# Optimization experiments

Hardware: AMD Instinct MI355X
Metric: run time of the kernel (lower is better)

## Reference

```python
import jax, jax.numpy as jnp
import numpy as np

FACTOR = 2
ALPHA = 0.1


def zero_upsample(x, f):
    # conv_transpose2d with one-hot (f,f) depthwise kernel == strided scatter
    N, C, H, W = x.shape
    out = jnp.zeros((N, C, H * f, W * f), dtype=x.dtype)
    return out.at[:, :, ::f, ::f].set(x)


def jitter_align(img, jitter, f):
    # pad by f on all sides (zeros), then per-batch crop shifted by floor(jitter*f)
    N, C, H, W = img.shape
    pad = jnp.pad(img, ((0, 0), (0, 0), (f, f), (f, f)))
    ji = jnp.floor(jitter * f).astype(jnp.int32)  # [N,2] = (x, y)
    def crop(im, jxy):
        i, j = jxy[1], jxy[0]
        return jax.lax.dynamic_slice(im, (0, f - i, f - j), (C, H, W))
    return jax.vmap(crop)(pad, ji)


def bilinear_upsample_jittered(img, jitter, f):
    # F.affine_grid(identity + translation) + grid_sample(bilinear,
    # align_corners=False, padding_mode='border')
    N, C, H, W = img.shape
    Ho, Wo = H * f, W * f
    xs = (2.0 * jnp.arange(Wo, dtype=img.dtype) + 1.0) / Wo - 1.0  # output pixel centers
    ys = (2.0 * jnp.arange(Ho, dtype=img.dtype) + 1.0) / Ho - 1.0
    def sample_one(im, jit):
        gx = xs + 2.0 * (0.5 - jit[0]) / W          # normalized grid x [Wo]
        gy = ys + 2.0 * (0.5 - jit[1]) / H          # normalized grid y [Ho]
        ix = ((gx + 1.0) * W - 1.0) / 2.0           # input pixel coords
        iy = ((gy + 1.0) * H - 1.0) / 2.0
        x0 = jnp.floor(ix)
        y0 = jnp.floor(iy)
        wx = (ix - x0)[None, None, :]               # [1,1,Wo]
        wy = (iy - y0)[None, :, None]               # [1,Ho,1]
        x0i = x0.astype(jnp.int32)
        y0i = y0.astype(jnp.int32)
        x0c = jnp.clip(x0i, 0, W - 1)
        x1c = jnp.clip(x0i + 1, 0, W - 1)
        y0c = jnp.clip(y0i, 0, H - 1)
        y1c = jnp.clip(y0i + 1, 0, H - 1)
        r0 = im[:, y0c, :]                          # [C,Ho,W]
        r1 = im[:, y1c, :]
        v00 = r0[:, :, x0c]; v01 = r0[:, :, x1c]    # [C,Ho,Wo]
        v10 = r1[:, :, x0c]; v11 = r1[:, :, x1c]
        top = v00 * (1 - wx) + v01 * wx
        bot = v10 * (1 - wx) + v11 * wx
        return top * (1 - wy) + bot * wy
    return jax.vmap(sample_one)(img, jitter)


def max_pool3(x):
    # 3x3 stride-1 max pool, pad 1 (torch pads with -inf for max pool)
    return jax.lax.reduce_window(x, -jnp.inf, jax.lax.max,
                                 (1, 1, 3, 3), (1, 1, 1, 1),
                                 [(0, 0), (0, 0), (1, 1), (1, 1)])


def nearest_up(x, f):
    return jnp.repeat(jnp.repeat(x, f, axis=2), f, axis=3)


def setup_inputs() -> dict:
    key = jax.random.key(0)
    k1, k2 = jax.random.split(key)
    frame = jax.random.uniform(k1, (4, 3, 540, 960), dtype=jnp.float32)
    jitter = jax.random.uniform(k2, (4, 2), dtype=jnp.float32)
    return {"frame": frame, "jitter": jitter}


def reference(frame, jitter):
    f = FACTOR
    N, C, H, W = frame.shape
    z_up = jitter_align(zero_upsample(frame, f), jitter, f)
    frame_bilinear = bilinear_upsample_jittered(frame, jitter, f)
    history = frame_bilinear  # first frame: history == None branch
    max_hr = nearest_up(max_pool3(frame), f)
    min_hr = nearest_up(-max_pool3(-frame), f)
    history = jnp.minimum(max_hr, history)
    history = jnp.maximum(min_hr, history)
    # beta has batch 1 in the original, so only jitter[0] is used for its align
    ones = jnp.ones((1, C, H, W), dtype=frame.dtype)
    beta = jitter_align(zero_upsample(ones, f), jitter[:1], f) * ALPHA
    return beta * z_up + (1 - beta) * history
```

## Files before the change

### kernel.cpp

```cpp
#include <hip/hip_runtime.h>
#include <math.h>

#define N_  4
#define C_  3
#define H_  540
#define W_  960
#define HO_ 1080
#define WO_ 1920

typedef float f32x4 __attribute__((ext_vector_type(4)));
typedef float f32x2 __attribute__((ext_vector_type(2)));

__global__ __launch_bounds__(256) void taa_fused_kernel(
    const float* __restrict__ frame,
    const float* __restrict__ jitter,
    float* __restrict__ out,
    int total_threads, int n_blocks, long long out_elems)
{
    int b   = blockIdx.x;
    int q   = n_blocks >> 3, r = n_blocks & 7;
    int xcd = b & 7, i = b >> 3;
    int wb  = (xcd < r ? xcd * (q + 1) : r * (q + 1) + (xcd - r) * q) + i;

    int idx = wb * 256 + threadIdx.x;
    if (idx >= total_threads) return;

    const int TX = W_ / 4;
    int tx  = idx % TX;
    int t   = idx / TX;
    int ly  = t % H_;
    int nc  = t / H_;
    int n   = nc / C_;
    int lx0 = tx * 4;

    float jx = jitter[2 * n + 0];
    float jy = jitter[2 * n + 1];
    int jnx = (int)floorf(jx * 2.0f);
    int jny = (int)floorf(jy * 2.0f);
    int bjx = (int)floorf(jitter[0] * 2.0f);
    int bjy = (int)floorf(jitter[1] * 2.0f);
    bool zcoin = (jnx == bjx) && (jny == bjy);

    const float* fp = frame + (size_t)nc * (H_ * W_);

    int r0 = (ly > 0)          ? ly - 1   : 0;
    int r2 = (ly < H_ - 1)     ? ly + 1   : H_ - 1;
    int cL = (lx0 > 0)         ? lx0 - 1  : 0;
    int cR = (lx0 + 4 < W_)    ? lx0 + 4  : W_ - 1;

    float w0[6], w1[6], w2[6];
    {
        const float* rp = fp + r0 * W_;
        f32x4 m = *(const f32x4*)(rp + lx0);
        w0[0]=rp[cL]; w0[1]=m.x; w0[2]=m.y; w0[3]=m.z; w0[4]=m.w; w0[5]=rp[cR];
        rp = fp + ly * W_;
        m = *(const f32x4*)(rp + lx0);
        w1[0]=rp[cL]; w1[1]=m.x; w1[2]=m.y; w1[3]=m.z; w1[4]=m.w; w1[5]=rp[cR];
        rp = fp + r2 * W_;
        m = *(const f32x4*)(rp + lx0);
        w2[0]=rp[cL]; w2[1]=m.x; w2[2]=m.y; w2[3]=m.z; w2[4]=m.w; w2[5]=rp[cR];
    }

    float cmax[6], cmin[6];
    #pragma unroll
    for (int j = 0; j < 6; ++j) {
        cmax[j] = fmaxf(fmaxf(w0[j], w1[j]), w2[j]);
        cmin[j] = fminf(fminf(w0[j], w1[j]), w2[j]);
    }
    float vmax[4], vmin[4];
    #pragma unroll
    for (int p = 0; p < 4; ++p) {
        vmax[p] = fmaxf(fmaxf(cmax[p], cmax[p+1]), cmax[p+2]);
        vmin[p] = fminf(fminf(cmin[p], cmin[p+1]), cmin[p+2]);
    }

    float wx_[2]; bool dxm1_[2];
    #pragma unroll
    for (int par = 0; par < 2; ++par) {
        int ox = 8 * tx + par;
        float xs = (2.0f * (float)ox + 1.0f) / (float)WO_ - 1.0f;
        float gx = xs + 2.0f * (0.5f - jx) / (float)W_;
        float ix = ((gx + 1.0f) * (float)W_ - 1.0f) / 2.0f;
        float x0f = floorf(ix);
        wx_[par]   = ix - x0f;
        dxm1_[par] = ((int)x0f < lx0);
    }
    f32x2 wx2 = { wx_[0], wx_[1] };

    size_t base = (size_t)nc * ((size_t)HO_ * WO_);

    #pragma unroll
    for (int ry = 0; ry < 2; ++ry) {
        int oy = 2 * ly + ry;
        float ysv = (2.0f * (float)oy + 1.0f) / (float)HO_ - 1.0f;
        float gy = ysv + 2.0f * (0.5f - jy) / (float)H_;
        float iy = ((gy + 1.0f) * (float)H_ - 1.0f) / 2.0f;
        float y0f = floorf(iy);
        float wy  = iy - y0f;
        bool up = ((int)y0f < ly);

        float brow[6];
        #pragma unroll
        for (int j = 0; j < 6; ++j) {
            float t0 = up ? w0[j] : w1[j];
            float t1 = up ? w1[j] : w2[j];
            brow[j] = t0 + wy * (t1 - t0);
        }
        float s0[5], s1[5];
        #pragma unroll
        for (int j = 0; j < 5; ++j) {
            s0[j] = dxm1_[0] ? brow[j] : brow[j + 1];
            s1[j] = dxm1_[1] ? brow[j] : brow[j + 1];
        }

        bool rowb = (ry == bjy);
        float res[8];
        #pragma unroll
        for (int bcol = 0; bcol < 4; ++bcol) {
            f32x2 v0 = { s0[bcol],     s1[bcol]     };
            f32x2 v1 = { s0[bcol + 1], s1[bcol + 1] };
            f32x2 bil = v0 + wx2 * (v1 - v0);
            f32x2 mx = { vmax[bcol], vmax[bcol] };
            f32x2 mn = { vmin[bcol], vmin[bcol] };
            f32x2 h  = __builtin_elementwise_max(mn, __builtin_elementwise_min(mx, bil));
            float zv = zcoin ? w1[bcol + 1] : 0.0f;
            res[2*bcol + 0] = (rowb && (bjx == 0)) ? (0.1f * zv + (1.0f - 0.1f) * h.x) : h.x;
            res[2*bcol + 1] = (rowb && (bjx == 1)) ? (0.1f * zv + (1.0f - 0.1f) * h.y) : h.y;
        }

        size_t off = base + (size_t)oy * WO_ + (size_t)8 * tx;
        if ((long long)(off + 8) <= out_elems) {
            f32x4 lo = { res[0], res[1], res[2], res[3] };
            f32x4 hi = { res[4], res[5], res[6], res[7] };
            *(f32x4*)(out + off)     = lo;
            *(f32x4*)(out + off + 4) = hi;
        }
    }
}

extern "C" void kernel_launch(void* const* d_in, const int* in_sizes, int n_in,
                              void* d_out, int out_size, void* d_ws, size_t ws_size,
                              hipStream_t stream) {
    const float* frame  = (const float*)d_in[0];
    const float* jitter = (const float*)d_in[1];
    float* out = (float*)d_out;

    const int total = N_ * C_ * H_ * (W_ / 4);
    const int block = 256;
    const int grid  = (total + block - 1) / block;
    taa_fused_kernel<<<grid, block, 0, stream>>>(frame, jitter, out,
                                                 total, grid, (long long)out_size);
}
```

Measured before the change: 28.04 us.

## Process four input rows per thread to reuse the vertical stencil window

Each thread now handles a 4x4 input tile and writes 8 output rows instead of 2, loading 6 input rows once rather than 3 rows per input row. Overlapping rows in the 3x3 min/max and bilinear stencil are shared across the four rows, which cuts redundant global loads and index arithmetic per output. In exchange there are a quarter as many threads, more registers per thread and less parallelism to hide store latency. It relies on H being divisible by 4 (540 is).

```diff
diff --git a/kernel.cpp b/kernel.cpp
--- a/kernel.cpp
+++ b/kernel.cpp
@@ -26,12 +26,14 @@
     if (idx >= total_threads) return;
 
     const int TX = W_ / 4;
+    const int HY = H_ / 4;
     int tx  = idx % TX;
     int t   = idx / TX;
-    int ly  = t % H_;
-    int nc  = t / H_;
+    int ly4 = t % HY;
+    int nc  = t / HY;
     int n   = nc / C_;
     int lx0 = tx * 4;
+    int ly0 = ly4 * 4;
 
     float jx = jitter[2 * n + 0];
     float jy = jitter[2 * n + 1];
@@ -43,35 +45,35 @@
 
     const float* fp = frame + (size_t)nc * (H_ * W_);
 
-    int r0 = (ly > 0)          ? ly - 1   : 0;
-    int r2 = (ly < H_ - 1)     ? ly + 1   : H_ - 1;
-    int cL = (lx0 > 0)         ? lx0 - 1  : 0;
-    int cR = (lx0 + 4 < W_)    ? lx0 + 4  : W_ - 1;
+    int cL = (lx0 > 0)      ? lx0 - 1 : 0;
+    int cR = (lx0 + 4 < W_) ? lx0 + 4 : W_ - 1;
 
-    float w0[6], w1[6], w2[6];
-    {
-        const float* rp = fp + r0 * W_;
+    float w[6][6];
+    #pragma unroll
+    for (int k = 0; k < 6; ++k) {
+        int row = ly0 - 1 + k;
+        row = (row < 0) ? 0 : ((row > H_ - 1) ? H_ - 1 : row);
+        const float* rp = fp + row * W_;
         f32x4 m = *(const f32x4*)(rp + lx0);
-        w0[0]=rp[cL]; w0[1]=m.x; w0[2]=m.y; w0[3]=m.z; w0[4]=m.w; w0[5]=rp[cR];
-        rp = fp + ly * W_;
-        m = *(const f32x4*)(rp + lx0);
-        w1[0]=rp[cL]; w1[1]=m.x; w1[2]=m.y; w1[3]=m.z; w1[4]=m.w; w1[5]=rp[cR];
-        rp = fp + r2 * W_;
-        m = *(const f32x4*)(rp + lx0);
-        w2[0]=rp[cL]; w2[1]=m.x; w2[2]=m.y; w2[3]=m.z; w2[4]=m.w; w2[5]=rp[cR];
+        w[k][0] = rp[cL];
+        w[k][1] = m.x; w[k][2] = m.y; w[k][3] = m.z; w[k][4] = m.w;
+        w[k][5] = rp[cR];
     }
 
-    float cmax[6], cmin[6];
+    float vmax[4][4], vmin[4][4];
     #pragma unroll
-    for (int j = 0; j < 6; ++j) {
-        cmax[j] = fmaxf(fmaxf(w0[j], w1[j]), w2[j]);
-        cmin[j] = fminf(fminf(w0[j], w1[j]), w2[j]);
-    }
-    float vmax[4], vmin[4];
-    #pragma unroll
-    for (int p = 0; p < 4; ++p) {
-        vmax[p] = fmaxf(fmaxf(cmax[p], cmax[p+1]), cmax[p+2]);
-        vmin[p] = fminf(fminf(cmin[p], cmin[p+1]), cmin[p+2]);
+    for (int h = 0; h < 4; ++h) {
+        float cmax[6], cmin[6];
+        #pragma unroll
+        for (int j = 0; j < 6; ++j) {
+            cmax[j] = fmaxf(fmaxf(w[h][j], w[h+1][j]), w[h+2][j]);
+            cmin[j] = fminf(fminf(w[h][j], w[h+1][j]), w[h+2][j]);
+        }
+        #pragma unroll
+        for (int p = 0; p < 4; ++p) {
+            vmax[h][p] = fmaxf(fmaxf(cmax[p], cmax[p+1]), cmax[p+2]);
+            vmin[h][p] = fminf(fminf(cmin[p], cmin[p+1]), cmin[p+2]);
+        }
     }
 
     float wx_[2]; bool dxm1_[2];
@@ -90,20 +92,22 @@
     size_t base = (size_t)nc * ((size_t)HO_ * WO_);
 
     #pragma unroll
-    for (int ry = 0; ry < 2; ++ry) {
-        int oy = 2 * ly + ry;
+    for (int ory = 0; ory < 8; ++ory) {
+        const int h = ory >> 1;
+        int lr = ly0 + h;
+        int oy = 8 * ly4 + ory;
         float ysv = (2.0f * (float)oy + 1.0f) / (float)HO_ - 1.0f;
         float gy = ysv + 2.0f * (0.5f - jy) / (float)H_;
         float iy = ((gy + 1.0f) * (float)H_ - 1.0f) / 2.0f;
         float y0f = floorf(iy);
         float wy  = iy - y0f;
-        bool up = ((int)y0f < ly);
+        bool up = ((int)y0f < lr);
 
         float brow[6];
         #pragma unroll
         for (int j = 0; j < 6; ++j) {
-            float t0 = up ? w0[j] : w1[j];
-            float t1 = up ? w1[j] : w2[j];
+            float t0 = up ? w[h][j]     : w[h+1][j];
+            float t1 = up ? w[h+1][j]   : w[h+2][j];
             brow[j] = t0 + wy * (t1 - t0);
         }
         float s0[5], s1[5];
@@ -113,19 +117,19 @@
             s1[j] = dxm1_[1] ? brow[j] : brow[j + 1];
         }
 
-        bool rowb = (ry == bjy);
+        bool rowb = ((ory & 1) == bjy);
         float res[8];
         #pragma unroll
         for (int bcol = 0; bcol < 4; ++bcol) {
             f32x2 v0 = { s0[bcol],     s1[bcol]     };
             f32x2 v1 = { s0[bcol + 1], s1[bcol + 1] };
             f32x2 bil = v0 + wx2 * (v1 - v0);
-            f32x2 mx = { vmax[bcol], vmax[bcol] };
-            f32x2 mn = { vmin[bcol], vmin[bcol] };
-            f32x2 h  = __builtin_elementwise_max(mn, __builtin_elementwise_min(mx, bil));
-            float zv = zcoin ? w1[bcol + 1] : 0.0f;
-            res[2*bcol + 0] = (rowb && (bjx == 0)) ? (0.1f * zv + (1.0f - 0.1f) * h.x) : h.x;
-            res[2*bcol + 1] = (rowb && (bjx == 1)) ? (0.1f * zv + (1.0f - 0.1f) * h.y) : h.y;
+            f32x2 mx = { vmax[h][bcol], vmax[h][bcol] };
+            f32x2 mn = { vmin[h][bcol], vmin[h][bcol] };
+            f32x2 hcl = __builtin_elementwise_max(mn, __builtin_elementwise_min(mx, bil));
+            float zv = zcoin ? w[h+1][bcol + 1] : 0.0f;
+            res[2*bcol + 0] = (rowb && (bjx == 0)) ? (0.1f * zv + (1.0f - 0.1f) * hcl.x) : hcl.x;
+            res[2*bcol + 1] = (rowb && (bjx == 1)) ? (0.1f * zv + (1.0f - 0.1f) * hcl.y) : hcl.y;
         }
 
         size_t off = base + (size_t)oy * WO_ + (size_t)8 * tx;
@@ -145,7 +149,7 @@
     const float* jitter = (const float*)d_in[1];
     float* out = (float*)d_out;
 
-    const int total = N_ * C_ * H_ * (W_ / 4);
+    const int total = N_ * C_ * (H_ / 4) * (W_ / 4);
     const int block = 256;
     const int grid  = (total + block - 1) / block;
     taa_fused_kernel<<<grid, block, 0, stream>>>(frame, jitter, out,
```

After: 27.22 us, median of 2. 1.03x faster.
